# Optimization experiments

Measured on AMD Instinct MI355X. Metric: run time of the kernel, lower is better.

## Reference

```python
import jax, jax.numpy as jnp
import numpy as np

L, E, M, F, P, C, NC = 12, 768, 256, 3072, 16, 3, 1000
IMG = 224
G = IMG // P          # 14 patches per side
NP = G * G            # 196 patches
B = 16


def setup_inputs() -> dict:
    key = jax.random.key(0)
    ks = jax.random.split(key, 10)
    s = 0.02
    return dict(
        x=jax.random.normal(ks[0], (B, C, IMG, IMG), jnp.float32),
        cls_tok=jax.random.normal(ks[1], (1, 1, E), jnp.float32),
        pos_emb=jax.random.normal(ks[2], (1, NP + 1, E), jnp.float32) * s,
        patch_w=jax.random.normal(ks[3], (E, C, P, P), jnp.float32) * s,
        patch_b=jnp.zeros((E,), jnp.float32),
        ln1_g=jnp.ones((L, E), jnp.float32), ln1_b=jnp.zeros((L, E), jnp.float32),
        proj=jax.random.normal(ks[4], (L, M, E), jnp.float32),  # Performer random features (buffer)
        ln2_g=jnp.ones((L, E), jnp.float32), ln2_b=jnp.zeros((L, E), jnp.float32),
        w1=jax.random.normal(ks[5], (L, E, F), jnp.float32) * s, b1=jnp.zeros((L, F), jnp.float32),
        w2=jax.random.normal(ks[6], (L, F, E), jnp.float32) * s, b2=jnp.zeros((L, E), jnp.float32),
        lnf_g=jnp.ones((E,), jnp.float32), lnf_b=jnp.zeros((E,), jnp.float32),
        head_w=jax.random.normal(ks[7], (E, NC), jnp.float32) * s,
        head_b=jnp.zeros((NC,), jnp.float32),
    )


def _ln(x, g, b):
    mu = jnp.mean(x, -1, keepdims=True)
    var = jnp.var(x, -1, keepdims=True)
    return (x - mu) * jax.lax.rsqrt(var + 1e-5) * g + b


def _performer(x, proj):
    # FaVOR+ softmax-kernel linear attention, non-causal, q=k=v=x. x:[B,N,E], proj:[M,E]
    d = x.shape[-1]
    m = proj.shape[0]
    xp = x * (d ** -0.25)                       # data normalizer d^{-1/4}
    logits = jnp.einsum('bne,me->bnm', xp, proj)
    diag = jnp.sum(xp * xp, -1, keepdims=True) * 0.5
    lg = logits - diag
    eps = 1e-4
    q_feat = jnp.exp(lg - jnp.max(lg, -1, keepdims=True)) * (m ** -0.5) + eps  # per-row max (queries)
    k_feat = jnp.exp(lg - jnp.max(lg)) * (m ** -0.5) + eps                     # global max (keys)
    kv = jnp.einsum('bnm,bne->bme', k_feat, x)                                 # [B,M,E]
    den = jnp.einsum('bnm,bm->bn', q_feat, jnp.sum(k_feat, axis=1))
    return jnp.einsum('bnm,bme->bne', q_feat, kv) / den[..., None]


def reference(x, cls_tok, pos_emb, patch_w, patch_b, ln1_g, ln1_b, proj,
              ln2_g, ln2_b, w1, b1, w2, b2, lnf_g, lnf_b, head_w, head_b):
    bsz = x.shape[0]
    # Conv2d(stride=kernel=P) patch embed == extract patches + matmul
    patches = x.reshape(bsz, C, G, P, G, P).transpose(0, 2, 4, 1, 3, 5).reshape(bsz, NP, C * P * P)
    tok = patches @ patch_w.reshape(E, C * P * P).T + patch_b          # [B,196,E]
    h = jnp.concatenate([jnp.broadcast_to(cls_tok, (bsz, 1, E)), tok], axis=1) + pos_emb

    def block(h, p):
        g1, b1_, pr, g2, b2_, W1, B1, W2, B2 = p
        h = h + _performer(_ln(h, g1, b1_), pr)
        m_in = _ln(h, g2, b2_)
        mlp = jax.nn.gelu(m_in @ W1 + B1, approximate=False) @ W2 + B2
        return h + mlp, None

    h, _ = jax.lax.scan(block, h, (ln1_g, ln1_b, proj, ln2_g, ln2_b, w1, b1, w2, b2))
    cls = _ln(h[:, 0], lnf_g, lnf_b)
    return cls @ head_w + head_b
```

## Files before the change

### kernel.cpp

```cpp
#include <hip/hip_runtime.h>
#include <math.h>

#define BSZ   16
#define NTOK  197
#define NPAT  196
#define EDIM  768
#define MDIM  256
#define FDIM  3072
#define NLAY  12
#define NCLS  1000
#define TTOT  (BSZ*NTOK)
#define TPAT  (BSZ*NPAT)
#define XSCALE 0.18995893f

typedef unsigned short ushortT;
typedef short s16x8 __attribute__((ext_vector_type(8)));
typedef float f32x4 __attribute__((ext_vector_type(4)));

__device__ __forceinline__ float4 ld4(const float* p) {
    return *reinterpret_cast<const float4*>(p);
}
__device__ __forceinline__ ushortT f2bf(float f) {
    unsigned u = __builtin_bit_cast(unsigned, f);
    unsigned r = (u + 0x7fff + ((u >> 16) & 1)) >> 16;
    return (ushortT)r;
}
__device__ __forceinline__ float bf2f(ushortT u) {
    return __builtin_bit_cast(float, ((unsigned)u) << 16);
}
__device__ __forceinline__ void load_lds16(const ushortT* g, ushortT* lds) {
    __builtin_amdgcn_global_load_lds(
        (const __attribute__((address_space(1))) unsigned int*)g,
        (__attribute__((address_space(3))) unsigned int*)lds, 16, 0, 0);
}

__global__ void gather_patches(const float* __restrict__ x, ushortT* __restrict__ patches) {
    int idx = blockIdx.x * 256 + threadIdx.x;
    if (idx >= TPAT * 768) return;
    int k = idx % 768;
    int t = idx / 768;
    int b = t / NPAT, p = t % NPAT;
    int c = k / 256, r = k % 256;
    int p1 = r / 16, p2 = r % 16;
    int g1 = p / 14, g2 = p % 14;
    patches[idx] = f2bf(x[(((size_t)b * 3 + c) * 224 + (g1 * 16 + p1)) * 224 + (g2 * 16 + p2)]);
}

__global__ void assemble_kernel(const float* __restrict__ tok, const float* __restrict__ cls_tok,
                                const float* __restrict__ pos, float* __restrict__ h) {
    int idx = blockIdx.x * 256 + threadIdx.x;
    int e = idx % 768;
    int t = idx / 768;
    int b = t / NTOK, n = t % NTOK;
    float v = (n == 0) ? cls_tok[e] : tok[((size_t)(b * NPAT + n - 1)) * 768 + e];
    h[idx] = v + pos[n * 768 + e];
}

__global__ void cvt_bf16(const float* __restrict__ in, ushortT* __restrict__ out, int n) {
    int idx = blockIdx.x * 256 + threadIdx.x;
    if (idx < n) out[idx] = f2bf(in[idx]);
}

__launch_bounds__(256)
__global__ void transpose_cvt(const float* __restrict__ in, ushortT* __restrict__ out,
                              int R, int Ccol) {
    __shared__ float tile[32][33];
    int c0 = blockIdx.x * 32, r0 = blockIdx.y * 32;
    int tx = threadIdx.x & 31, ty = threadIdx.x >> 5;
    #pragma unroll
    for (int i = 0; i < 32; i += 8)
        tile[ty + i][tx] = in[(size_t)(r0 + ty + i) * Ccol + c0 + tx];
    __syncthreads();
    #pragma unroll
    for (int i = 0; i < 32; i += 8)
        out[(size_t)(c0 + ty + i) * R + r0 + tx] = f2bf(tile[tx][ty + i]);
}

template<int EPI>
__launch_bounds__(256)
__global__ void mgemm(const ushortT* __restrict__ A, const ushortT* __restrict__ Bt,
                      const float* __restrict__ bias, float* __restrict__ C,
                      ushortT* __restrict__ Cb, int M, int N, int K) {
    __shared__ ushortT As[128 * 32];
    __shared__ ushortT Bs[128 * 32];
    const int t = threadIdx.x;
    const int n0 = blockIdx.x * 128;
    const int m0 = blockIdx.y * 128;
    const int lane = t & 63;
    const int wv = t >> 6;
    const int wm = (wv >> 1) * 64;
    const int wn = (wv & 1) * 64;
    f32x4 acc[4][4];
    #pragma unroll
    for (int i = 0; i < 4; ++i)
        #pragma unroll
        for (int j = 0; j < 4; ++j) acc[i][j] = (f32x4)0.f;

    const ushortT* aptr = A + (size_t)(m0 + (t >> 2)) * K + (t & 3) * 8;
    const ushortT* bptr = Bt + (size_t)(n0 + (t >> 2)) * K + (t & 3) * 8;
    ushortT* aLds = As + t * 8;
    ushortT* bLds = Bs + t * 8;
    const size_t rowStep = (size_t)64 * K;

    const int fr = lane & 15;
    const int fko = (lane >> 4) * 8;
    const ushortT* aRd = As + (wm + fr) * 32 + fko;
    const ushortT* bRd = Bs + (wn + fr) * 32 + fko;

    for (int k0 = 0; k0 < K; k0 += 32) {
        load_lds16(aptr, aLds);
        load_lds16(aptr + rowStep, aLds + 2048);
        load_lds16(bptr, bLds);
        load_lds16(bptr + rowStep, bLds + 2048);
        aptr += 32; bptr += 32;
        __syncthreads();
        s16x8 af[4], bfr[4];
        #pragma unroll
        for (int i = 0; i < 4; ++i) af[i] = *(const s16x8*)(aRd + i * 512);
        #pragma unroll
        for (int j = 0; j < 4; ++j) bfr[j] = *(const s16x8*)(bRd + j * 512);
        #pragma unroll
        for (int i = 0; i < 4; ++i)
            #pragma unroll
            for (int j = 0; j < 4; ++j)
                acc[i][j] = __builtin_amdgcn_mfma_f32_16x16x32_bf16(af[i], bfr[j], acc[i][j], 0, 0, 0);
        __syncthreads();
    }

    const int orow = (lane >> 4) * 4;
    const int ocol = lane & 15;
    #pragma unroll
    for (int i = 0; i < 4; ++i) {
        #pragma unroll
        for (int r = 0; r < 4; ++r) {
            int row = m0 + wm + i * 16 + orow + r;
            if (row >= M) continue;
            #pragma unroll
            for (int j = 0; j < 4; ++j) {
                int col = n0 + wn + j * 16 + ocol;
                float v = acc[i][j][r] + bias[col];
                size_t o = (size_t)row * N + col;
                if (EPI == 0) {
                    C[o] = v;
                } else if (EPI == 1) {
                    v = 0.5f * v * (1.0f + erff(v * 0.70710678118f));
                    Cb[o] = f2bf(v);
                } else {
                    C[o] = C[o] + v;
                }
            }
        }
    }
}

__launch_bounds__(256)
__global__ void gemm64_lg(const float* __restrict__ A, const float* __restrict__ Bm,
                          const float* __restrict__ diag, float* __restrict__ Cd,
                          int Mrows, int Ncols, int Kdim) {
    __shared__ float As[16][64];
    __shared__ float Bs[16][64];
    const int tid = threadIdx.x;
    const int n0 = blockIdx.x * 64;
    const int m0 = blockIdx.y * 64;
    const int tx = tid & 15, ty = tid >> 4;
    float acc[4][4] = {};
    const int lr = tid >> 2;
    const int lc = (tid & 3) << 2;
    for (int k0 = 0; k0 < Kdim; k0 += 16) {
        float4 av = make_float4(0.f, 0.f, 0.f, 0.f);
        int ar = m0 + lr;
        if (ar < Mrows) av = ld4(A + (size_t)ar * Kdim + k0 + lc);
        As[lc + 0][lr] = av.x; As[lc + 1][lr] = av.y;
        As[lc + 2][lr] = av.z; As[lc + 3][lr] = av.w;
        int bn = tid >> 2;
        int bk = (tid & 3) << 2;
        float4 bv = ld4(Bm + (size_t)(n0 + bn) * Kdim + k0 + bk);
        Bs[bk + 0][bn] = bv.x; Bs[bk + 1][bn] = bv.y;
        Bs[bk + 2][bn] = bv.z; Bs[bk + 3][bn] = bv.w;
        __syncthreads();
        #pragma unroll
        for (int k = 0; k < 16; ++k) {
            float a[4], bb[4];
            #pragma unroll
            for (int i = 0; i < 4; ++i) a[i] = As[k][ty * 4 + i];
            #pragma unroll
            for (int j = 0; j < 4; ++j) bb[j] = Bs[k][tx * 4 + j];
            #pragma unroll
            for (int i = 0; i < 4; ++i)
                #pragma unroll
                for (int j = 0; j < 4; ++j)
                    acc[i][j] += a[i] * bb[j];
        }
        __syncthreads();
    }
    #pragma unroll
    for (int i = 0; i < 4; ++i) {
        int row = m0 + ty * 4 + i;
        if (row >= Mrows) continue;
        #pragma unroll
        for (int j = 0; j < 4; ++j) {
            int col = n0 + tx * 4 + j;
            Cd[(size_t)row * Ncols + col] = acc[i][j] * XSCALE - diag[row];
        }
    }
}

__launch_bounds__(256)
__global__ void ln_kernel(const float* __restrict__ in, int rowStride,
                          const float* __restrict__ g, const float* __restrict__ b,
                          float* __restrict__ out, ushortT* __restrict__ outb,
                          float* __restrict__ diag) {
    int row = blockIdx.x;
    const float* xr = in + (size_t)row * rowStride;
    int tid = threadIdx.x;
    float v0 = xr[tid], v1 = xr[tid + 256], v2 = xr[tid + 512];
    float s = v0 + v1 + v2;
    float q = v0 * v0 + v1 * v1 + v2 * v2;
    int lane = tid & 63, wid = tid >> 6;
    #pragma unroll
    for (int off = 32; off >= 1; off >>= 1) {
        s += __shfl_down(s, off);
        q += __shfl_down(q, off);
    }
    __shared__ float sh[8];
    __shared__ float mu_s, rs_s;
    if (lane == 0) { sh[wid] = s; sh[4 + wid] = q; }
    __syncthreads();
    if (tid == 0) {
        float ts = sh[0] + sh[1] + sh[2] + sh[3];
        float tq = sh[4] + sh[5] + sh[6] + sh[7];
        float mu = ts * (1.0f / 768.0f);
        float var = tq * (1.0f / 768.0f) - mu * mu;
        mu_s = mu;
        rs_s = rsqrtf(var + 1e-5f);
    }
    __syncthreads();
    float mu = mu_s, rs = rs_s;
    float y0 = (v0 - mu) * rs * g[tid] + b[tid];
    float y1 = (v1 - mu) * rs * g[tid + 256] + b[tid + 256];
    float y2 = (v2 - mu) * rs * g[tid + 512] + b[tid + 512];
    size_t o = (size_t)row * 768;
    out[o + tid] = y0;
    out[o + tid + 256] = y1;
    out[o + tid + 512] = y2;
    outb[o + tid] = f2bf(y0);
    outb[o + tid + 256] = f2bf(y1);
    outb[o + tid + 512] = f2bf(y2);
    if (diag) {
        float qq = y0 * y0 + y1 * y1 + y2 * y2;
        #pragma unroll
        for (int off = 32; off >= 1; off >>= 1) qq += __shfl_down(qq, off);
        if (lane == 0) sh[wid] = qq;
        __syncthreads();
        if (tid == 0) diag[row] = 0.5f * XSCALE * XSCALE * (sh[0] + sh[1] + sh[2] + sh[3]);
    }
}

__launch_bounds__(64)
__global__ void rowmax_kernel(const float* __restrict__ lg, float* __restrict__ rmax) {
    int row = blockIdx.x;
    int lane = threadIdx.x;
    const float* r = lg + (size_t)row * 256;
    float m = fmaxf(fmaxf(r[lane], r[lane + 64]), fmaxf(r[lane + 128], r[lane + 192]));
    #pragma unroll
    for (int off = 32; off >= 1; off >>= 1) m = fmaxf(m, __shfl_down(m, off));
    if (lane == 0) rmax[row] = m;
}

__launch_bounds__(256)
__global__ void gmax_kernel(const float* __restrict__ rmax, float* __restrict__ gmax) {
    int tid = threadIdx.x;
    float m = -1e30f;
    for (int i = tid; i < TTOT; i += 256) m = fmaxf(m, rmax[i]);
    int lane = tid & 63, wid = tid >> 6;
    #pragma unroll
    for (int off = 32; off >= 1; off >>= 1) m = fmaxf(m, __shfl_down(m, off));
    __shared__ float sh[4];
    if (lane == 0) sh[wid] = m;
    __syncthreads();
    if (tid == 0) gmax[0] = fmaxf(fmaxf(sh[0], sh[1]), fmaxf(sh[2], sh[3]));
}

__global__ void feat_kernel(const float* __restrict__ lg, const float* __restrict__ rmax,
                            const float* __restrict__ gmax, float* __restrict__ qf,
                            float* __restrict__ kf) {
    int idx = blockIdx.x * 256 + threadIdx.x;
    int row = idx >> 8;
    float v = lg[idx];
    qf[idx] = expf(v - rmax[row]) * 0.0625f + 1e-4f;
    kf[idx] = expf(v - gmax[0]) * 0.0625f + 1e-4f;
}

__launch_bounds__(256)
__global__ void kv_kernel(const float* __restrict__ kf, const float* __restrict__ xln,
                          float* __restrict__ kv, float* __restrict__ ksum) {
    int blk = blockIdx.x;
    int b = blk >> 5;
    int m0 = (blk & 31) << 3;
    __shared__ float kc[NTOK * 8];
    int tid = threadIdx.x;
    for (int i = tid; i < NTOK * 8; i += 256) {
        int n = i >> 3, j = i & 7;
        kc[i] = kf[((size_t)(b * NTOK + n)) * 256 + m0 + j];
    }
    __syncthreads();
    if (tid < 8) {
        float s = 0.f;
        for (int n = 0; n < NTOK; ++n) s += kc[n * 8 + tid];
        ksum[b * 256 + m0 + tid] = s;
    }
    float acc[8][3] = {};
    const float* xb = xln + (size_t)b * NTOK * 768;
    for (int n = 0; n < NTOK; ++n) {
        float x0 = xb[n * 768 + tid];
        float x1 = xb[n * 768 + tid + 256];
        float x2 = xb[n * 768 + tid + 512];
        #pragma unroll
        for (int j = 0; j < 8; ++j) {
            float kk = kc[n * 8 + j];
            acc[j][0] += kk * x0;
            acc[j][1] += kk * x1;
            acc[j][2] += kk * x2;
        }
    }
    float* kvb = kv + ((size_t)b * 256 + m0) * 768;
    #pragma unroll
    for (int j = 0; j < 8; ++j) {
        kvb[j * 768 + tid] = acc[j][0];
        kvb[j * 768 + tid + 256] = acc[j][1];
        kvb[j * 768 + tid + 512] = acc[j][2];
    }
}

__launch_bounds__(256)
__global__ void att_kernel(const float* __restrict__ qf, const float* __restrict__ ksum,
                           const float* __restrict__ kv, float* __restrict__ h) {
    int blk = blockIdx.x;
    int b = blk / 25;
    int n0 = (blk % 25) * 8;
    int nrows = NTOK - n0; if (nrows > 8) nrows = 8;
    __shared__ float qs[8][256];
    __shared__ float dinv[8];
    __shared__ float sh[4];
    int tid = threadIdx.x;
    for (int r = 0; r < nrows; ++r)
        qs[r][tid] = qf[((size_t)(b * NTOK + n0 + r)) * 256 + tid];
    for (int r = nrows; r < 8; ++r) qs[r][tid] = 0.f;
    __syncthreads();
    int lane = tid & 63, wid = tid >> 6;
    float ks = ksum[b * 256 + tid];
    for (int r = 0; r < nrows; ++r) {
        float d = qs[r][tid] * ks;
        #pragma unroll
        for (int off = 32; off >= 1; off >>= 1) d += __shfl_down(d, off);
        if (lane == 0) sh[wid] = d;
        __syncthreads();
        if (tid == 0) dinv[r] = 1.0f / (sh[0] + sh[1] + sh[2] + sh[3]);
        __syncthreads();
    }
    float acc[8][3] = {};
    const float* kvb = kv + (size_t)b * 256 * 768;
    for (int m = 0; m < 256; ++m) {
        float k0 = kvb[m * 768 + tid];
        float k1 = kvb[m * 768 + tid + 256];
        float k2 = kvb[m * 768 + tid + 512];
        #pragma unroll
        for (int r = 0; r < 8; ++r) {
            float qv = qs[r][m];
            acc[r][0] += qv * k0;
            acc[r][1] += qv * k1;
            acc[r][2] += qv * k2;
        }
    }
    for (int r = 0; r < nrows; ++r) {
        float di = dinv[r];
        size_t o = ((size_t)(b * NTOK + n0 + r)) * 768;
        h[o + tid]       += acc[r][0] * di;
        h[o + tid + 256] += acc[r][1] * di;
        h[o + tid + 512] += acc[r][2] * di;
    }
}

__global__ void head_kernel(const float* __restrict__ cls, const float* __restrict__ w,
                            const float* __restrict__ hb, float* __restrict__ out) {
    int idx = blockIdx.x * 256 + threadIdx.x;
    if (idx >= BSZ * NCLS) return;
    int i = idx / NCLS, j = idx % NCLS;
    float acc = hb[j];
    const float* cr = cls + (size_t)i * 768;
    for (int k = 0; k < 768; ++k) acc += cr[k] * w[k * NCLS + j];
    out[idx] = acc;
}

extern "C" void kernel_launch(void* const* d_in, const int* in_sizes, int n_in,
                              void* d_out, int out_size, void* d_ws, size_t ws_size,
                              hipStream_t stream) {
    const float* x       = (const float*)d_in[0];
    const float* cls_tok = (const float*)d_in[1];
    const float* pos_emb = (const float*)d_in[2];
    const float* patch_w = (const float*)d_in[3];
    const float* patch_b = (const float*)d_in[4];
    const float* ln1_g   = (const float*)d_in[5];
    const float* ln1_b   = (const float*)d_in[6];
    const float* proj    = (const float*)d_in[7];
    const float* ln2_g   = (const float*)d_in[8];
    const float* ln2_b   = (const float*)d_in[9];
    const float* w1      = (const float*)d_in[10];
    const float* b1      = (const float*)d_in[11];
    const float* w2      = (const float*)d_in[12];
    const float* b2      = (const float*)d_in[13];
    const float* lnf_g   = (const float*)d_in[14];
    const float* lnf_b   = (const float*)d_in[15];
    const float* head_w  = (const float*)d_in[16];
    const float* head_b  = (const float*)d_in[17];
    float* out = (float*)d_out;

    char* wsb = (char*)d_ws;
    ushortT* y1b        = (ushortT*)wsb;
    float*   tok        = (float*)wsb;
    ushortT* patches_bf = (ushortT*)(wsb + 9633792);
    size_t off = 19660800;
    float*   h      = (float*)(wsb + off); off += 9682944;
    float*   xln    = (float*)(wsb + off); off += 9830400;
    ushortT* xln_bf = (ushortT*)(wsb + off); off += 4915200;
    float*   lg     = (float*)(wsb + off); off += 3227648;
    float*   qf     = (float*)(wsb + off); off += 3227648;
    float*   kf     = (float*)(wsb + off); off += 3227648;
    float*   kv     = (float*)(wsb + off); off += 12582912;
    ushortT* w1t    = (ushortT*)(wsb + off); off += 4718592;
    ushortT* w2t    = (ushortT*)(wsb + off); off += 4718592;
    ushortT* pwb    = (ushortT*)(wsb + off); off += 1179648;
    float*   diag   = (float*)(wsb + off); off += 12800;
    float*   rmax   = (float*)(wsb + off); off += 12800;
    float*   gmaxp  = (float*)(wsb + off); off += 256;
    float*   ksum   = (float*)(wsb + off); off += 16384;
    float*   clsln  = (float*)(wsb + off); off += 49152;

    gather_patches<<<9408, 256, 0, stream>>>(x, patches_bf);
    cvt_bf16<<<2304, 256, 0, stream>>>(patch_w, pwb, 768 * 768);
    mgemm<0><<<dim3(6, 25), 256, 0, stream>>>(patches_bf, pwb, patch_b, tok, nullptr,
                                              TPAT, 768, 768);
    assemble_kernel<<<9456, 256, 0, stream>>>(tok, cls_tok, pos_emb, h);

    for (int l = 0; l < NLAY; ++l) {
        transpose_cvt<<<dim3(96, 24), 256, 0, stream>>>(w1 + (size_t)l * 768 * FDIM, w1t, 768, FDIM);
        transpose_cvt<<<dim3(24, 96), 256, 0, stream>>>(w2 + (size_t)l * FDIM * 768, w2t, FDIM, 768);

        ln_kernel<<<TTOT, 256, 0, stream>>>(h, 768, ln1_g + l * 768, ln1_b + l * 768,
                                            xln, xln_bf, diag);
        gemm64_lg<<<dim3(4, 50), 256, 0, stream>>>(xln, proj + (size_t)l * 256 * 768,
                                                   diag, lg, TTOT, 256, 768);
        rowmax_kernel<<<TTOT, 64, 0, stream>>>(lg, rmax);
        gmax_kernel<<<1, 256, 0, stream>>>(rmax, gmaxp);
        feat_kernel<<<TTOT, 256, 0, stream>>>(lg, rmax, gmaxp, qf, kf);
        kv_kernel<<<BSZ * 32, 256, 0, stream>>>(kf, xln, kv, ksum);
        att_kernel<<<BSZ * 25, 256, 0, stream>>>(qf, ksum, kv, h);
        ln_kernel<<<TTOT, 256, 0, stream>>>(h, 768, ln2_g + l * 768, ln2_b + l * 768,
                                            xln, xln_bf, nullptr);
        mgemm<1><<<dim3(24, 25), 256, 0, stream>>>(xln_bf, w1t, b1 + l * FDIM,
                                                   nullptr, y1b, TTOT, FDIM, 768);
        mgemm<2><<<dim3(6, 25), 256, 0, stream>>>(y1b, w2t, b2 + l * 768,
                                                  h, nullptr, TTOT, 768, FDIM);
    }

    ln_kernel<<<BSZ, 256, 0, stream>>>(h, NTOK * 768, lnf_g, lnf_b, clsln, xln_bf, nullptr);
    head_kernel<<<(BSZ * NCLS + 255) / 256, 256, 0, stream>>>(clsln, head_w, head_b, out);
}
```

Baseline: 3.798 ms.

## Fuse performer feature kernels, batch weight transposes, and add 64-tile FFN2 GEMM

Replaces the rowmax/gmax/feat kernels with one row kernel that computes query features and updates a per-layer global max through an ordered-integer atomicMax. The key features are now recomputed inside kv_kernel. LayerNorm2 is fused into the attention epilogue, and the bf16 copy from LN1 is dropped. All layers' weight transposes run in one batched launch up front when the workspace is large enough. The second MLP GEMM moves to a 64x64 tile kernel that launches more blocks, trading some reuse for better CU occupancy. Together these cut launch count and intermediate traffic, with extra exp work in kv_kernel and atomic contention as the costs.

After: 3.690 ms. 2.8% less time.

```diff
diff --git a/kernel.cpp b/kernel.cpp
--- a/kernel.cpp
+++ b/kernel.cpp
@@ -25,13 +25,18 @@
     unsigned r = (u + 0x7fff + ((u >> 16) & 1)) >> 16;
     return (ushortT)r;
 }
-__device__ __forceinline__ float bf2f(ushortT u) {
-    return __builtin_bit_cast(float, ((unsigned)u) << 16);
-}
 __device__ __forceinline__ void load_lds16(const ushortT* g, ushortT* lds) {
     __builtin_amdgcn_global_load_lds(
         (const __attribute__((address_space(1))) unsigned int*)g,
         (__attribute__((address_space(3))) unsigned int*)lds, 16, 0, 0);
+}
+__device__ __forceinline__ unsigned fenc(float f) {
+    unsigned u = __builtin_bit_cast(unsigned, f);
+    return u ^ ((u >> 31) ? 0xFFFFFFFFu : 0x80000000u);
+}
+__device__ __forceinline__ float fdec(unsigned u) {
+    u ^= ((u >> 31) ? 0x80000000u : 0xFFFFFFFFu);
+    return __builtin_bit_cast(float, u);
 }
 
 __global__ void gather_patches(const float* __restrict__ x, ushortT* __restrict__ patches) {
@@ -61,19 +66,26 @@
     if (idx < n) out[idx] = f2bf(in[idx]);
 }
 
+__global__ void init_gmax(unsigned* __restrict__ g) {
+    if (threadIdx.x < NLAY) g[threadIdx.x] = 0u;
+}
+
 __launch_bounds__(256)
 __global__ void transpose_cvt(const float* __restrict__ in, ushortT* __restrict__ out,
                               int R, int Ccol) {
+    size_t elems = (size_t)R * Ccol;
+    const float* ip = in + (size_t)blockIdx.z * elems;
+    ushortT* op = out + (size_t)blockIdx.z * elems;
     __shared__ float tile[32][33];
     int c0 = blockIdx.x * 32, r0 = blockIdx.y * 32;
     int tx = threadIdx.x & 31, ty = threadIdx.x >> 5;
     #pragma unroll
     for (int i = 0; i < 32; i += 8)
-        tile[ty + i][tx] = in[(size_t)(r0 + ty + i) * Ccol + c0 + tx];
+        tile[ty + i][tx] = ip[(size_t)(r0 + ty + i) * Ccol + c0 + tx];
     __syncthreads();
     #pragma unroll
     for (int i = 0; i < 32; i += 8)
-        out[(size_t)(c0 + ty + i) * R + r0 + tx] = f2bf(tile[tx][ty + i]);
+        op[(size_t)(c0 + ty + i) * R + r0 + tx] = f2bf(tile[tx][ty + i]);
 }
 
 template<int EPI>
@@ -142,12 +154,76 @@
                 size_t o = (size_t)row * N + col;
                 if (EPI == 0) {
                     C[o] = v;
-                } else if (EPI == 1) {
+                } else {
                     v = 0.5f * v * (1.0f + erff(v * 0.70710678118f));
                     Cb[o] = f2bf(v);
-                } else {
-                    C[o] = C[o] + v;
                 }
+            }
+        }
+    }
+}
+
+__launch_bounds__(256)
+__global__ void mgemm64(const ushortT* __restrict__ A, const ushortT* __restrict__ Bt,
+                        const float* __restrict__ bias, float* __restrict__ C,
+                        int M, int N, int K) {
+    __shared__ ushortT As[64 * 32];
+    __shared__ ushortT Bs[64 * 32];
+    const int t = threadIdx.x;
+    const int n0 = blockIdx.x * 64;
+    const int m0 = blockIdx.y * 64;
+    const int lane = t & 63;
+    const int wv = t >> 6;
+    const int wm = (wv >> 1) * 32;
+    const int wn = (wv & 1) * 32;
+    f32x4 acc[2][2];
+    #pragma unroll
+    for (int i = 0; i < 2; ++i)
+        #pragma unroll
+        for (int j = 0; j < 2; ++j) acc[i][j] = (f32x4)0.f;
+
+    const ushortT* aptr = A + (size_t)(m0 + (t >> 2)) * K + (t & 3) * 8;
+    const ushortT* bptr = Bt + (size_t)(n0 + (t >> 2)) * K + (t & 3) * 8;
+    ushortT* aLds = As + t * 8;
+    ushortT* bLds = Bs + t * 8;
+
+    const int fr = lane & 15;
+    const int fko = (lane >> 4) * 8;
+    const ushortT* aRd = As + (wm + fr) * 32 + fko;
+    const ushortT* bRd = Bs + (wn + fr) * 32 + fko;
+
+    for (int k0 = 0; k0 < K; k0 += 32) {
+        load_lds16(aptr, aLds);
+        load_lds16(bptr, bLds);
+        aptr += 32; bptr += 32;
+        __syncthreads();
+        s16x8 af[2], bfr[2];
+        #pragma unroll
+        for (int i = 0; i < 2; ++i) af[i] = *(const s16x8*)(aRd + i * 512);
+        #pragma unroll
+        for (int j = 0; j < 2; ++j) bfr[j] = *(const s16x8*)(bRd + j * 512);
+        #pragma unroll
+        for (int i = 0; i < 2; ++i)
+            #pragma unroll
+            for (int j = 0; j < 2; ++j)
+                acc[i][j] = __builtin_amdgcn_mfma_f32_16x16x32_bf16(af[i], bfr[j], acc[i][j], 0, 0, 0);
+        __syncthreads();
+    }
+
+    const int orow = (lane >> 4) * 4;
+    const int ocol = lane & 15;
+    #pragma unroll
+    for (int i = 0; i < 2; ++i) {
+        #pragma unroll
+        for (int r = 0; r < 4; ++r) {
+            int row = m0 + wm + i * 16 + orow + r;
+            if (row >= M) continue;
+            #pragma unroll
+            for (int j = 0; j < 2; ++j) {
+                int col = n0 + wn + j * 16 + ocol;
+                float v = acc[i][j][r] + bias[col];
+                size_t o = (size_t)row * N + col;
+                C[o] = C[o] + v;
             }
         }
     }
@@ -243,9 +319,11 @@
     out[o + tid] = y0;
     out[o + tid + 256] = y1;
     out[o + tid + 512] = y2;
-    outb[o + tid] = f2bf(y0);
-    outb[o + tid + 256] = f2bf(y1);
-    outb[o + tid + 512] = f2bf(y2);
+    if (outb) {
+        outb[o + tid] = f2bf(y0);
+        outb[o + tid + 256] = f2bf(y1);
+        outb[o + tid + 512] = f2bf(y2);
+    }
     if (diag) {
         float qq = y0 * y0 + y1 * y1 + y2 * y2;
         #pragma unroll
@@ -256,52 +334,43 @@
     }
 }
 
-__launch_bounds__(64)
-__global__ void rowmax_kernel(const float* __restrict__ lg, float* __restrict__ rmax) {
+__launch_bounds__(256)
+__global__ void rowqf_kernel(const float* __restrict__ lg, float* __restrict__ qf,
+                             unsigned* __restrict__ gslot) {
     int row = blockIdx.x;
-    int lane = threadIdx.x;
-    const float* r = lg + (size_t)row * 256;
-    float m = fmaxf(fmaxf(r[lane], r[lane + 64]), fmaxf(r[lane + 128], r[lane + 192]));
-    #pragma unroll
-    for (int off = 32; off >= 1; off >>= 1) m = fmaxf(m, __shfl_down(m, off));
-    if (lane == 0) rmax[row] = m;
-}
-
-__launch_bounds__(256)
-__global__ void gmax_kernel(const float* __restrict__ rmax, float* __restrict__ gmax) {
     int tid = threadIdx.x;
-    float m = -1e30f;
-    for (int i = tid; i < TTOT; i += 256) m = fmaxf(m, rmax[i]);
+    float v = lg[(size_t)row * 256 + tid];
+    float m = v;
     int lane = tid & 63, wid = tid >> 6;
     #pragma unroll
     for (int off = 32; off >= 1; off >>= 1) m = fmaxf(m, __shfl_down(m, off));
     __shared__ float sh[4];
+    __shared__ float bm_s;
     if (lane == 0) sh[wid] = m;
     __syncthreads();
-    if (tid == 0) gmax[0] = fmaxf(fmaxf(sh[0], sh[1]), fmaxf(sh[2], sh[3]));
-}
-
-__global__ void feat_kernel(const float* __restrict__ lg, const float* __restrict__ rmax,
-                            const float* __restrict__ gmax, float* __restrict__ qf,
-                            float* __restrict__ kf) {
-    int idx = blockIdx.x * 256 + threadIdx.x;
-    int row = idx >> 8;
-    float v = lg[idx];
-    qf[idx] = expf(v - rmax[row]) * 0.0625f + 1e-4f;
-    kf[idx] = expf(v - gmax[0]) * 0.0625f + 1e-4f;
-}
-
-__launch_bounds__(256)
-__global__ void kv_kernel(const float* __restrict__ kf, const float* __restrict__ xln,
+    if (tid == 0) {
+        float bm = fmaxf(fmaxf(sh[0], sh[1]), fmaxf(sh[2], sh[3]));
+        bm_s = bm;
+        atomicMax(gslot, fenc(bm));
+    }
+    __syncthreads();
+    qf[(size_t)row * 256 + tid] = expf(v - bm_s) * 0.0625f + 1e-4f;
+}
+
+__launch_bounds__(256)
+__global__ void kv_kernel(const float* __restrict__ lg, const unsigned* __restrict__ gslot,
+                          const float* __restrict__ xln,
                           float* __restrict__ kv, float* __restrict__ ksum) {
     int blk = blockIdx.x;
     int b = blk >> 5;
     int m0 = (blk & 31) << 3;
     __shared__ float kc[NTOK * 8];
     int tid = threadIdx.x;
+    float gm = fdec(*gslot);
     for (int i = tid; i < NTOK * 8; i += 256) {
         int n = i >> 3, j = i & 7;
-        kc[i] = kf[((size_t)(b * NTOK + n)) * 256 + m0 + j];
+        float lv = lg[((size_t)(b * NTOK + n)) * 256 + m0 + j];
+        kc[i] = expf(lv - gm) * 0.0625f + 1e-4f;
     }
     __syncthreads();
     if (tid < 8) {
@@ -333,15 +402,18 @@
 }
 
 __launch_bounds__(256)
-__global__ void att_kernel(const float* __restrict__ qf, const float* __restrict__ ksum,
-                           const float* __restrict__ kv, float* __restrict__ h) {
+__global__ void att_ln2(const float* __restrict__ qf, const float* __restrict__ ksum,
+                        const float* __restrict__ kv, float* __restrict__ h,
+                        const float* __restrict__ lng, const float* __restrict__ lnb,
+                        ushortT* __restrict__ xlnbf) {
     int blk = blockIdx.x;
     int b = blk / 25;
     int n0 = (blk % 25) * 8;
     int nrows = NTOK - n0; if (nrows > 8) nrows = 8;
     __shared__ float qs[8][256];
     __shared__ float dinv[8];
-    __shared__ float sh[4];
+    __shared__ float sh[8];
+    __shared__ float mu_s, rs_s;
     int tid = threadIdx.x;
     for (int r = 0; r < nrows; ++r)
         qs[r][tid] = qf[((size_t)(b * NTOK + n0 + r)) * 256 + tid];
@@ -372,12 +444,36 @@
             acc[r][2] += qv * k2;
         }
     }
+    float g0 = lng[tid], g1 = lng[tid + 256], g2 = lng[tid + 512];
+    float c0 = lnb[tid], c1 = lnb[tid + 256], c2 = lnb[tid + 512];
     for (int r = 0; r < nrows; ++r) {
         float di = dinv[r];
         size_t o = ((size_t)(b * NTOK + n0 + r)) * 768;
-        h[o + tid]       += acc[r][0] * di;
-        h[o + tid + 256] += acc[r][1] * di;
-        h[o + tid + 512] += acc[r][2] * di;
+        float h0 = h[o + tid]       + acc[r][0] * di;
+        float h1 = h[o + tid + 256] + acc[r][1] * di;
+        float h2 = h[o + tid + 512] + acc[r][2] * di;
+        h[o + tid] = h0; h[o + tid + 256] = h1; h[o + tid + 512] = h2;
+        float s = h0 + h1 + h2;
+        float q = h0 * h0 + h1 * h1 + h2 * h2;
+        #pragma unroll
+        for (int off = 32; off >= 1; off >>= 1) {
+            s += __shfl_down(s, off);
+            q += __shfl_down(q, off);
+        }
+        if (lane == 0) { sh[wid] = s; sh[4 + wid] = q; }
+        __syncthreads();
+        if (tid == 0) {
+            float ts = sh[0] + sh[1] + sh[2] + sh[3];
+            float tq = sh[4] + sh[5] + sh[6] + sh[7];
+            float mu = ts * (1.0f / 768.0f);
+            mu_s = mu;
+            rs_s = rsqrtf(tq * (1.0f / 768.0f) - mu * mu + 1e-5f);
+        }
+        __syncthreads();
+        float mu = mu_s, rs = rs_s;
+        xlnbf[o + tid]       = f2bf((h0 - mu) * rs * g0 + c0);
+        xlnbf[o + tid + 256] = f2bf((h1 - mu) * rs * g1 + c1);
+        xlnbf[o + tid + 512] = f2bf((h2 - mu) * rs * g2 + c2);
     }
 }
 
@@ -420,21 +516,29 @@
     float*   tok        = (float*)wsb;
     ushortT* patches_bf = (ushortT*)(wsb + 9633792);
     size_t off = 19660800;
-    float*   h      = (float*)(wsb + off); off += 9682944;
-    float*   xln    = (float*)(wsb + off); off += 9830400;
-    ushortT* xln_bf = (ushortT*)(wsb + off); off += 4915200;
-    float*   lg     = (float*)(wsb + off); off += 3227648;
-    float*   qf     = (float*)(wsb + off); off += 3227648;
-    float*   kf     = (float*)(wsb + off); off += 3227648;
-    float*   kv     = (float*)(wsb + off); off += 12582912;
-    ushortT* w1t    = (ushortT*)(wsb + off); off += 4718592;
-    ushortT* w2t    = (ushortT*)(wsb + off); off += 4718592;
-    ushortT* pwb    = (ushortT*)(wsb + off); off += 1179648;
-    float*   diag   = (float*)(wsb + off); off += 12800;
-    float*   rmax   = (float*)(wsb + off); off += 12800;
-    float*   gmaxp  = (float*)(wsb + off); off += 256;
-    float*   ksum   = (float*)(wsb + off); off += 16384;
-    float*   clsln  = (float*)(wsb + off); off += 49152;
+    float*    h      = (float*)(wsb + off);    off += 9682944;
+    float*    xln    = (float*)(wsb + off);    off += 9830400;
+    ushortT*  xln_bf = (ushortT*)(wsb + off);  off += 4915200;
+    float*    lg     = (float*)(wsb + off);    off += 3227648;
+    float*    qf     = (float*)(wsb + off);    off += 3227648;
+    float*    kv     = (float*)(wsb + off);    off += 12582912;
+    ushortT*  pwb    = (ushortT*)(wsb + off);  off += 1179648;
+    float*    diag   = (float*)(wsb + off);    off += 12800;
+    unsigned* gml    = (unsigned*)(wsb + off); off += 256;
+    float*    ksum   = (float*)(wsb + off);    off += 16384;
+    float*    clsln  = (float*)(wsb + off);    off += 49152;
+    const size_t WSTRIDE = (size_t)3072 * 768;
+    ushortT*  w1t    = (ushortT*)(wsb + off);
+    bool big = ws_size >= off + 2u * NLAY * WSTRIDE * sizeof(ushortT);
+    size_t w1bytes = (big ? NLAY : 1) * WSTRIDE * sizeof(ushortT);
+    ushortT*  w2t    = (ushortT*)(wsb + off + w1bytes);
+
+    init_gmax<<<1, 64, 0, stream>>>(gml);
+
+    if (big) {
+        transpose_cvt<<<dim3(96, 24, NLAY), 256, 0, stream>>>(w1, w1t, 768, FDIM);
+        transpose_cvt<<<dim3(24, 96, NLAY), 256, 0, stream>>>(w2, w2t, FDIM, 768);
+    }
 
     gather_patches<<<9408, 256, 0, stream>>>(x, patches_bf);
     cvt_bf16<<<2304, 256, 0, stream>>>(patch_w, pwb, 768 * 768);
@@ -443,26 +547,27 @@
     assemble_kernel<<<9456, 256, 0, stream>>>(tok, cls_tok, pos_emb, h);
 
     for (int l = 0; l < NLAY; ++l) {
-        transpose_cvt<<<dim3(96, 24), 256, 0, stream>>>(w1 + (size_t)l * 768 * FDIM, w1t, 768, FDIM);
-        transpose_cvt<<<dim3(24, 96), 256, 0, stream>>>(w2 + (size_t)l * FDIM * 768, w2t, FDIM, 768);
+        ushortT* w1l = big ? w1t + (size_t)l * WSTRIDE : w1t;
+        ushortT* w2l = big ? w2t + (size_t)l * WSTRIDE : w2t;
+        if (!big) {
+            transpose_cvt<<<dim3(96, 24), 256, 0, stream>>>(w1 + (size_t)l * WSTRIDE, w1l, 768, FDIM);
+            transpose_cvt<<<dim3(24, 96), 256, 0, stream>>>(w2 + (size_t)l * WSTRIDE, w2l, FDIM, 768);
+        }
 
         ln_kernel<<<TTOT, 256, 0, stream>>>(h, 768, ln1_g + l * 768, ln1_b + l * 768,
-                                            xln, xln_bf, diag);
+                                            xln, nullptr, diag);
         gemm64_lg<<<dim3(4, 50), 256, 0, stream>>>(xln, proj + (size_t)l * 256 * 768,
                                                    diag, lg, TTOT, 256, 768);
-        rowmax_kernel<<<TTOT, 64, 0, stream>>>(lg, rmax);
-        gmax_kernel<<<1, 256, 0, stream>>>(rmax, gmaxp);
-        feat_kernel<<<TTOT, 256, 0, stream>>>(lg, rmax, gmaxp, qf, kf);
-        kv_kernel<<<BSZ * 32, 256, 0, stream>>>(kf, xln, kv, ksum);
-        att_kernel<<<BSZ * 25, 256, 0, stream>>>(qf, ksum, kv, h);
-        ln_kernel<<<TTOT, 256, 0, stream>>>(h, 768, ln2_g + l * 768, ln2_b + l * 768,
-                                            xln, xln_bf, nullptr);
-        mgemm<1><<<dim3(24, 25), 256, 0, stream>>>(xln_bf, w1t, b1 + l * FDIM,
+        rowqf_kernel<<<TTOT, 256, 0, stream>>>(lg, qf, gml + l);
+        kv_kernel<<<BSZ * 32, 256, 0, stream>>>(lg, gml + l, xln, kv, ksum);
+        att_ln2<<<BSZ * 25, 256, 0, stream>>>(qf, ksum, kv, h,
+                                              ln2_g + l * 768, ln2_b + l * 768, xln_bf);
+        mgemm<1><<<dim3(24, 25), 256, 0, stream>>>(xln_bf, w1l, b1 + l * FDIM,
                                                    nullptr, y1b, TTOT, FDIM, 768);
-        mgemm<2><<<dim3(6, 25), 256, 0, stream>>>(y1b, w2t, b2 + l * 768,
-                                                  h, nullptr, TTOT, 768, FDIM);
-    }
-
-    ln_kernel<<<BSZ, 256, 0, stream>>>(h, NTOK * 768, lnf_g, lnf_b, clsln, xln_bf, nullptr);
+        mgemm64<<<dim3(12, 50), 256, 0, stream>>>(y1b, w2l, b2 + l * 768,
+                                                  h, TTOT, 768, FDIM);
+    }
+
+    ln_kernel<<<BSZ, 256, 0, stream>>>(h, NTOK * 768, lnf_g, lnf_b, clsln, nullptr, nullptr);
     head_kernel<<<(BSZ * NCLS + 255) / 256, 256, 0, stream>>>(clsln, head_w, head_b, out);
 }
```
